# Optimization experiments

Hardware: AMD Instinct MI355X
Metric: run time of the kernel (lower is better)

The kernel has to match this reference:

```python
import jax, jax.numpy as jnp
import numpy as np

B, E, WIN, DX, DZ, RAW = 2048, 32, 10, 14, 14, 22

def _leaky(x):
    return jnp.where(x >= 0, x, 0.01 * x)

def setup_inputs():
    key = jax.random.key(0)
    ks = jax.random.split(key, 20)
    def w(k, i, o):
        return jax.random.normal(k, (i, o), dtype=jnp.float32) / np.float32(np.sqrt(i))
    def b(k, o):
        return jax.random.normal(k, (o,), dtype=jnp.float32) * 0.01
    return {
        "raw_obs": jax.random.normal(ks[0], (B, WIN, 1, RAW), dtype=jnp.float32),
        "state_prev": jax.random.normal(ks[1], (B, E, WIN, DX), dtype=jnp.float32),
        "pm_w1": w(ks[2], WIN * DX, 256), "pm_b1": b(ks[3], 256),
        "pm_w3": w(ks[4], 256, 512), "pm_b3": b(ks[5], 512),
        "pm_wm2": w(ks[6], 512, DX), "pm_bm2": b(ks[7], DX),
        "sm_w2": w(ks[8], WIN * RAW, 256), "sm_b2": b(ks[9], 256),
        "sm_w3": w(ks[10], 256, 256), "sm_b3": b(ks[11], 256),
        "sm_w5": w(ks[12], 256, 64), "sm_b5": b(ks[13], 64),
        "sm_w6": w(ks[14], 64, DZ), "sm_b6": b(ks[15], DZ),
        "on_w1": w(ks[16], DZ, 32), "on_b1": b(ks[17], 32),
        "on_w2": w(ks[18], 32, DZ), "on_b2": b(ks[19], DZ),
    }

def reference(raw_obs, state_prev, pm_w1, pm_b1, pm_w3, pm_b3, pm_wm2, pm_bm2,
              sm_w2, sm_b2, sm_w3, sm_b3, sm_w5, sm_b5, sm_w6, sm_b6,
              on_w1, on_b1, on_w2, on_b2):
    bs, ens, win, dx = state_prev.shape
    dz = sm_w6.shape[1]
    # --- process model (LinearFlipout evaluated at mean weights) ---
    x = state_prev.reshape(bs * ens, win * dx)
    x = _leaky(x @ pm_w1 + pm_b1)
    x = _leaky(x @ pm_w3 + pm_b3)
    state_pred = (x @ pm_wm2 + pm_bm2).reshape(bs, ens, dx)   # [B,E,dx]
    state_m = state_pred.mean(axis=1)                          # [B,dx]
    A = state_pred - state_m[:, None, :]                       # [B,E,dx]
    # --- sensor model: torch repeat(E,1,1,1) tiles ensemble-major, the final
    # reshape reinterprets as batch-major; replicate that layout faithfully ---
    s = jnp.tile(raw_obs, (ens, 1, 1, 1)).reshape(bs * ens, win * raw_obs.shape[-1])
    s = _leaky(s @ sm_w2 + sm_b2)
    s = _leaky(s @ sm_w3 + sm_b3)
    s = _leaky(s @ sm_w5 + sm_b5)
    s = s @ sm_w6 + sm_b6
    ensemble_z = s.reshape(bs, ens, dz)                        # [B,E,dz]
    z = ensemble_z.mean(axis=1, keepdims=True)                 # [B,1,dz]
    # --- observation noise R = diag_embed(square(mlp(z)+c) + init) ---
    r = jax.nn.relu(z @ on_w1 + on_b1) @ on_w2 + on_b2
    r = jnp.square(r + 0.001) + 0.038729833
    R = r.reshape(bs, dz)[:, :, None] * jnp.eye(dz, dtype=r.dtype)  # [B,dz,dz]
    # --- EnKF correction ---
    S = jnp.einsum('bei,bej->bij', A, A)                       # AT @ A, [B,dx,dx]
    innovation = S / (ens - 1) + R
    K = (S / (ens - 1)) @ jnp.linalg.inv(innovation)           # [B,dx,dz]
    diff = ensemble_z - state_pred                             # (y - H_XT)^T, [B,E,dz]
    gain = jnp.einsum('bij,bej->bei', K, diff)                 # [B,E,dx]
    state_corrected = state_pred + gain
    return (state_corrected,
            state_corrected.mean(axis=1, keepdims=True),
            state_m[:, None, :],
            z,
            ensemble_z)
```

## Files before the change

kernel.cpp:

```cpp
#include <hip/hip_runtime.h>

typedef unsigned short u16;
typedef __attribute__((ext_vector_type(8))) short short8;
typedef __attribute__((ext_vector_type(4))) float floatx4;

#define MFMA_BF16 __builtin_amdgcn_mfma_f32_16x16x32_bf16

__device__ __forceinline__ u16 f2bf(float f) {
    union { float f; unsigned int i; } v; v.f = f;
    unsigned int u = v.i;
    u += 0x7fffu + ((u >> 16) & 1u);
    return (u16)(u >> 16);
}
__device__ __forceinline__ float leaky(float x) { return x >= 0.f ? x : 0.01f * x; }

#define H1S 264
#define RS 232
#define H3S 72
#define CS 136

#define O1 917504
#define O2 946176
#define O3 974848
#define O4 1003520

#define PW1   0
#define PW3   40960
#define PWM2  172032
#define PSW2  180224
#define PSW3  237568
#define PSW5  303104
#define PSW6  319488
#define PTOTAL 320512
#define WS_NEEDED 641024
#define WS_BIG (641024 + 3670016)

struct PackSeg { const float* W; int K, N, S, base, count; };
struct PackArgs { PackSeg seg[7]; };

__global__ __launch_bounds__(256) void pack_all(PackArgs pa, u16* __restrict__ P) {
    int u = blockIdx.x * 256 + threadIdx.x;
    if (u >= PTOTAL) return;
#pragma unroll
    for (int i = 0; i < 7; i++) {
        if (u >= pa.seg[i].base && u < pa.seg[i].base + pa.seg[i].count) {
            int v = u - pa.seg[i].base;
            int j = v & 7;
            int l = (v >> 3) & 63;
            int ts = v >> 9;
            int s = ts % pa.seg[i].S;
            int t = ts / pa.seg[i].S;
            int k = s * 32 + (l >> 4) * 8 + j;
            int n = t * 16 + (l & 15);
            P[u] = (k < pa.seg[i].K && n < pa.seg[i].N)
                       ? f2bf(pa.seg[i].W[k * pa.seg[i].N + n]) : (u16)0;
            return;
        }
    }
}

__device__ __forceinline__ short8 load_x_frag(const float* __restrict__ X,
                                              int row, int s, int q) {
    const float* p = X + row * 140;
    float4 v0 = {0.f, 0.f, 0.f, 0.f}, v1 = {0.f, 0.f, 0.f, 0.f};
    int col0 = s * 32 + q * 8;
    if (s < 4) {
        v0 = *(const float4*)(p + col0);
        v1 = *(const float4*)(p + col0 + 4);
    } else {
        if (q <= 1) v0 = *(const float4*)(p + col0);
        if (q == 0) v1 = *(const float4*)(p + col0 + 4);
    }
    short8 r;
    r[0] = (short)f2bf(v0.x); r[1] = (short)f2bf(v0.y);
    r[2] = (short)f2bf(v0.z); r[3] = (short)f2bf(v0.w);
    r[4] = (short)f2bf(v1.x); r[5] = (short)f2bf(v1.y);
    r[6] = (short)f2bf(v1.z); r[7] = (short)f2bf(v1.w);
    return r;
}

__global__ __launch_bounds__(256, 5) void merged_mlp(
    const float* __restrict__ Rg, const float* __restrict__ Xg,
    const u16* __restrict__ Pk,
    const float* __restrict__ b1, const float* __restrict__ b3,
    const float* __restrict__ bm2,
    const float* __restrict__ b2, const float* __restrict__ sb3,
    const float* __restrict__ b5, const float* __restrict__ b6,
    float* __restrict__ ez_out,
    float* __restrict__ sp_ws)
{
    __shared__ __align__(16) u16 ldsH[32 * H1S];
    __shared__ __align__(16) u16 ldsC[32 * CS];

    const int tid  = threadIdx.x;
    const int lane = tid & 63;
    const int wave = tid >> 6;
    const int q    = lane >> 4;
    const int n16  = lane & 15;

    if (blockIdx.x < 64) {
        const u16* w2p = Pk + PSW2;
        const u16* w3p = Pk + PSW3;
        const u16* w5p = Pk + PSW5;
        const u16* w6p = Pk + PSW6;
        const int row0 = blockIdx.x * 32;

        for (int idx = tid; idx < 32 * 56; idx += 256) {
            int r = idx / 56, c4 = idx - r * 56;
            float4 v = {0.f, 0.f, 0.f, 0.f};
            if (c4 < 55) v = *(const float4*)&Rg[(row0 + r) * 220 + c4 * 4];
            u16* dst = &ldsH[r * RS + c4 * 4];
            dst[0] = f2bf(v.x); dst[1] = f2bf(v.y); dst[2] = f2bf(v.z); dst[3] = f2bf(v.w);
        }
        __syncthreads();

        floatx4 acc1[2][4];
        {
            floatx4 zero = {0.f, 0.f, 0.f, 0.f};
            for (int rt = 0; rt < 2; rt++)
                for (int ct = 0; ct < 4; ct++) acc1[rt][ct] = zero;
#pragma unroll
            for (int s = 0; s < 7; s++) {
                short8 a0 = *(const short8*)&ldsH[n16 * RS + s * 32 + q * 8];
                short8 a1 = *(const short8*)&ldsH[(n16 + 16) * RS + s * 32 + q * 8];
#pragma unroll
                for (int ct = 0; ct < 4; ct++) {
                    int t = wave * 4 + ct;
                    short8 bf = *(const short8*)&w2p[((t * 7 + s) * 64 + lane) * 8];
                    acc1[0][ct] = MFMA_BF16(a0, bf, acc1[0][ct], 0, 0, 0);
                    acc1[1][ct] = MFMA_BF16(a1, bf, acc1[1][ct], 0, 0, 0);
                }
            }
        }
        __syncthreads();
#pragma unroll
        for (int ct = 0; ct < 4; ct++) {
            int col = (wave * 4 + ct) * 16 + n16;
            float bias = b2[col];
#pragma unroll
            for (int rt = 0; rt < 2; rt++)
#pragma unroll
                for (int r = 0; r < 4; r++)
                    ldsH[(rt * 16 + q * 4 + r) * H1S + col] = f2bf(leaky(acc1[rt][ct][r] + bias));
        }
        __syncthreads();

        floatx4 acc5[2];
        {
            floatx4 zero = {0.f, 0.f, 0.f, 0.f};
            acc5[0] = zero; acc5[1] = zero;
        }
#pragma unroll
        for (int c = 0; c < 2; c++) {
            floatx4 zero = {0.f, 0.f, 0.f, 0.f};
            floatx4 acc[2][2];
            for (int rt = 0; rt < 2; rt++)
                for (int ct = 0; ct < 2; ct++) acc[rt][ct] = zero;
#pragma unroll
            for (int s = 0; s < 8; s++) {
                short8 a0 = *(const short8*)&ldsH[n16 * H1S + s * 32 + q * 8];
                short8 a1 = *(const short8*)&ldsH[(n16 + 16) * H1S + s * 32 + q * 8];
#pragma unroll
                for (int ct = 0; ct < 2; ct++) {
                    int tg = c * 8 + wave * 2 + ct;
                    short8 bf = *(const short8*)&w3p[((tg * 8 + s) * 64 + lane) * 8];
                    acc[0][ct] = MFMA_BF16(a0, bf, acc[0][ct], 0, 0, 0);
                    acc[1][ct] = MFMA_BF16(a1, bf, acc[1][ct], 0, 0, 0);
                }
            }
#pragma unroll
            for (int ct = 0; ct < 2; ct++) {
                int cl = (wave * 2 + ct) * 16 + n16;
                float bias = sb3[c * 128 + cl];
#pragma unroll
                for (int rt = 0; rt < 2; rt++)
#pragma unroll
                    for (int r = 0; r < 4; r++)
                        ldsC[(rt * 16 + q * 4 + r) * CS + cl] = f2bf(leaky(acc[rt][ct][r] + bias));
            }
            __syncthreads();
#pragma unroll
            for (int sl = 0; sl < 4; sl++) {
                int sg = c * 4 + sl;
                short8 bf = *(const short8*)&w5p[((wave * 8 + sg) * 64 + lane) * 8];
#pragma unroll
                for (int rt = 0; rt < 2; rt++) {
                    short8 a = *(const short8*)&ldsC[(rt * 16 + n16) * CS + sl * 32 + q * 8];
                    acc5[rt] = MFMA_BF16(a, bf, acc5[rt], 0, 0, 0);
                }
            }
            __syncthreads();
        }

        {
            int col = wave * 16 + n16;
            float bias = b5[col];
#pragma unroll
            for (int rt = 0; rt < 2; rt++)
#pragma unroll
                for (int r = 0; r < 4; r++)
                    ldsC[(rt * 16 + q * 4 + r) * H3S + col] = f2bf(leaky(acc5[rt][r] + bias));
        }
        __syncthreads();

        if (wave < 2) {
            floatx4 zero = {0.f, 0.f, 0.f, 0.f};
            floatx4 acc[2] = {zero, zero};
            int s = wave;
            short8 a0 = *(const short8*)&ldsC[n16 * H3S + s * 32 + q * 8];
            short8 a1 = *(const short8*)&ldsC[(n16 + 16) * H3S + s * 32 + q * 8];
            short8 bf = *(const short8*)&w6p[(s * 64 + lane) * 8];
            acc[0] = MFMA_BF16(a0, bf, acc[0], 0, 0, 0);
            acc[1] = MFMA_BF16(a1, bf, acc[1], 0, 0, 0);
            float* pacc = (float*)ldsH;
#pragma unroll
            for (int rt = 0; rt < 2; rt++)
#pragma unroll
                for (int r = 0; r < 4; r++)
                    pacc[(wave * 32 + rt * 16 + q * 4 + r) * 16 + n16] = acc[rt][r];
        }
        __syncthreads();
        {
            const float* pacc = (const float*)ldsH;
            for (int idx = tid; idx < 512; idx += 256) {
                int r = idx >> 4, c = idx & 15;
                float v = pacc[idx] + pacc[512 + idx];
                if (c < 14) ez_out[(row0 + r) * 14 + c] = v + b6[c];
            }
        }
    } else {
        const u16* w1p  = Pk + PW1;
        const u16* w3p  = Pk + PW3;
        const u16* wm2p = Pk + PWM2;
        const int bb   = blockIdx.x - 64;
        const int row0 = bb * 32;

        {
            floatx4 zero = {0.f, 0.f, 0.f, 0.f};
            floatx4 acc[2][4];
            for (int rt = 0; rt < 2; rt++)
                for (int ct = 0; ct < 4; ct++) acc[rt][ct] = zero;
#pragma unroll
            for (int s = 0; s < 5; s++) {
                short8 a0 = load_x_frag(Xg, row0 + n16, s, q);
                short8 a1 = load_x_frag(Xg, row0 + 16 + n16, s, q);
#pragma unroll
                for (int ct = 0; ct < 4; ct++) {
                    int t = wave * 4 + ct;
                    short8 bf = *(const short8*)&w1p[((t * 5 + s) * 64 + lane) * 8];
                    acc[0][ct] = MFMA_BF16(a0, bf, acc[0][ct], 0, 0, 0);
                    acc[1][ct] = MFMA_BF16(a1, bf, acc[1][ct], 0, 0, 0);
                }
            }
#pragma unroll
            for (int ct = 0; ct < 4; ct++) {
                int col = (wave * 4 + ct) * 16 + n16;
                float bias = b1[col];
#pragma unroll
                for (int rt = 0; rt < 2; rt++)
#pragma unroll
                    for (int r = 0; r < 4; r++)
                        ldsH[(rt * 16 + q * 4 + r) * H1S + col] = f2bf(leaky(acc[rt][ct][r] + bias));
            }
        }
        __syncthreads();

        floatx4 acc3[2];
        {
            floatx4 zero = {0.f, 0.f, 0.f, 0.f};
            acc3[0] = zero; acc3[1] = zero;
        }
#pragma unroll
        for (int c = 0; c < 4; c++) {
            floatx4 zero = {0.f, 0.f, 0.f, 0.f};
            floatx4 acc[2][2];
            for (int rt = 0; rt < 2; rt++)
                for (int ct = 0; ct < 2; ct++) acc[rt][ct] = zero;
#pragma unroll
            for (int s = 0; s < 8; s++) {
                short8 a0 = *(const short8*)&ldsH[n16 * H1S + s * 32 + q * 8];
                short8 a1 = *(const short8*)&ldsH[(n16 + 16) * H1S + s * 32 + q * 8];
#pragma unroll
                for (int ct = 0; ct < 2; ct++) {
                    int tg = c * 8 + wave * 2 + ct;
                    short8 bf = *(const short8*)&w3p[((tg * 8 + s) * 64 + lane) * 8];
                    acc[0][ct] = MFMA_BF16(a0, bf, acc[0][ct], 0, 0, 0);
                    acc[1][ct] = MFMA_BF16(a1, bf, acc[1][ct], 0, 0, 0);
                }
            }
#pragma unroll
            for (int ct = 0; ct < 2; ct++) {
                int cl = (wave * 2 + ct) * 16 + n16;
                float bias = b3[c * 128 + cl];
#pragma unroll
                for (int rt = 0; rt < 2; rt++)
#pragma unroll
                    for (int r = 0; r < 4; r++)
                        ldsC[(rt * 16 + q * 4 + r) * CS + cl] = f2bf(leaky(acc[rt][ct][r] + bias));
            }
            __syncthreads();
            {
                int sg = c * 4 + wave;
                short8 bf = *(const short8*)&wm2p[(sg * 64 + lane) * 8];
#pragma unroll
                for (int rt = 0; rt < 2; rt++) {
                    short8 a = *(const short8*)&ldsC[(rt * 16 + n16) * CS + wave * 32 + q * 8];
                    acc3[rt] = MFMA_BF16(a, bf, acc3[rt], 0, 0, 0);
                }
            }
            __syncthreads();
        }

        {
            float* pacc = (float*)ldsH;
#pragma unroll
            for (int rt = 0; rt < 2; rt++)
#pragma unroll
                for (int r = 0; r < 4; r++)
                    pacc[(wave * 32 + rt * 16 + q * 4 + r) * 16 + n16] = acc3[rt][r];
        }
        __syncthreads();
        {
            const float* pacc = (const float*)ldsH;
            for (int idx = tid; idx < 512; idx += 256) {
                int r = idx >> 4, c = idx & 15;
                float v = pacc[idx] + pacc[512 + idx] + pacc[1024 + idx] + pacc[1536 + idx];
                if (c < 14) sp_ws[(row0 + r) * 14 + c] = v + bm2[c];
            }
        }
    }
}

__global__ __launch_bounds__(64) void enkf_tail(
    const float* __restrict__ sp_all,
    const float* __restrict__ on_w1, const float* __restrict__ on_b1,
    const float* __restrict__ on_w2, const float* __restrict__ on_b2,
    float* out)
{
    __shared__ float spv[32][14];
    __shared__ float ezv[32][14];
    __shared__ float smv[14], zzv[14], rrv[14];
    __shared__ float M[14][14], Kmat[14][14];
    __shared__ float G[14][28];
    __shared__ float fac[14];
    __shared__ float hbuf[32];

    const int l = threadIdx.x;
    const int b = blockIdx.x;

    for (int idx = l; idx < 448; idx += 64) ((float*)spv)[idx] = sp_all[b * 448 + idx];
    {
        const float* ezsrc = out + O4 + (b & 63) * 448;
        for (int idx = l; idx < 448; idx += 64) ((float*)ezv)[idx] = ezsrc[idx];
    }

    if (l < 14) {
        float s1 = 0.f, s2 = 0.f;
        for (int e = 0; e < 32; e++) { s1 += spv[e][l]; s2 += ezv[e][l]; }
        smv[l] = s1 * (1.f / 32.f);
        zzv[l] = s2 * (1.f / 32.f);
    }
    if (l < 32) {
        float t = on_b1[l];
        for (int k = 0; k < 14; k++) t += zzv[k] * on_w1[k * 32 + l];
        hbuf[l] = t > 0.f ? t : 0.f;
    }
    if (l < 14) {
        float t = on_b2[l];
        for (int k = 0; k < 32; k++) t += hbuf[k] * on_w2[k * 14 + l];
        t += 0.001f;
        rrv[l] = t * t + 0.038729833f;
    }
    for (int idx = l; idx < 196; idx += 64) {
        int i = idx / 14, j = idx - i * 14;
        float s = 0.f;
        for (int e = 0; e < 32; e++) s += (spv[e][i] - smv[i]) * (spv[e][j] - smv[j]);
        s *= (1.f / 31.f);
        M[i][j] = s;
        G[i][j] = s + (i == j ? rrv[i] : 0.f);
        G[i][14 + j] = (i == j) ? 1.f : 0.f;
    }
    for (int c = 0; c < 14; c++) {
        float pinv = 1.f / G[c][c];
        if (l < 28) G[c][l] *= pinv;
        if (l < 14 && l != c) fac[l] = G[l][c];
        for (int idx = l; idx < 392; idx += 64) {
            int i = idx / 28, j = idx - i * 28;
            if (i != c) G[i][j] -= fac[i] * G[c][j];
        }
    }
    for (int idx = l; idx < 196; idx += 64) {
        int i = idx / 14, j = idx - i * 14;
        float s = 0.f;
        for (int k = 0; k < 14; k++) s += M[i][k] * G[k][14 + j];
        Kmat[i][j] = s;
    }
    for (int idx = l; idx < 448; idx += 64) {
        int e = idx / 14, i = idx - e * 14;
        float g = 0.f;
        for (int j = 0; j < 14; j++) g += Kmat[i][j] * (ezv[e][j] - spv[e][j]);
        out[b * 448 + idx] = spv[e][i] + g;
        out[O4 + b * 448 + idx] = ezv[e][i];
    }
    if (l < 14) {
        float g = 0.f;
        for (int j = 0; j < 14; j++) g += Kmat[l][j] * (zzv[j] - smv[j]);
        out[O1 + b * 14 + l] = smv[l] + g;
        out[O2 + b * 14 + l] = smv[l];
        out[O3 + b * 14 + l] = zzv[l];
    }
}

extern "C" void kernel_launch(void* const* d_in, const int* in_sizes, int n_in,
                              void* d_out, int out_size, void* d_ws, size_t ws_size,
                              hipStream_t stream) {
    (void)in_sizes; (void)n_in; (void)out_size; (void)ws_size;

    const float* raw_obs    = (const float*)d_in[0];
    const float* state_prev = (const float*)d_in[1];
    const float* pm_w1  = (const float*)d_in[2];
    const float* pm_b1  = (const float*)d_in[3];
    const float* pm_w3  = (const float*)d_in[4];
    const float* pm_b3  = (const float*)d_in[5];
    const float* pm_wm2 = (const float*)d_in[6];
    const float* pm_bm2 = (const float*)d_in[7];
    const float* sm_w2  = (const float*)d_in[8];
    const float* sm_b2  = (const float*)d_in[9];
    const float* sm_w3  = (const float*)d_in[10];
    const float* sm_b3  = (const float*)d_in[11];
    const float* sm_w5  = (const float*)d_in[12];
    const float* sm_b5  = (const float*)d_in[13];
    const float* sm_w6  = (const float*)d_in[14];
    const float* sm_b6  = (const float*)d_in[15];
    const float* on_w1  = (const float*)d_in[16];
    const float* on_b1  = (const float*)d_in[17];
    const float* on_w2  = (const float*)d_in[18];
    const float* on_b2  = (const float*)d_in[19];

    float* out = (float*)d_out;
    u16* P = (u16*)d_ws;
    float* sp_ws = (float*)((char*)d_ws + WS_NEEDED);

    PackArgs pa;
    pa.seg[0] = { pm_w1,  140, 256, 5,  PW1,  40960  };
    pa.seg[1] = { pm_w3,  256, 512, 8,  PW3,  131072 };
    pa.seg[2] = { pm_wm2, 512, 14,  16, PWM2, 8192   };
    pa.seg[3] = { sm_w2,  220, 256, 7,  PSW2, 57344  };
    pa.seg[4] = { sm_w3,  256, 256, 8,  PSW3, 65536  };
    pa.seg[5] = { sm_w5,  256, 64,  8,  PSW5, 16384  };
    pa.seg[6] = { sm_w6,  64,  14,  2,  PSW6, 1024   };
    pack_all<<<(PTOTAL + 255) / 256, 256, 0, stream>>>(pa, P);

    merged_mlp<<<2112, 256, 0, stream>>>(raw_obs, state_prev, P,
                                         pm_b1, pm_b3, pm_bm2,
                                         sm_b2, sm_b3, sm_b5, sm_b6,
                                         out + O4, sp_ws);
    enkf_tail<<<2048, 64, 0, stream>>>(sp_ws, on_w1, on_b1, on_w2, on_b2, out);
}
```

Baseline: 183.1 us.

## Widen LDS hidden-layer staging to full width and cut chunk barriers

The intermediate LDS buffer grows to the full 256-wide hidden row. The sensor model's second layer is now computed in one pass, ping-ponging between two buffers, and layer 5 runs as a single K=256 reduction instead of being interleaved over two chunks. The process model's 512-wide layer now uses two 256-column chunks instead of four 128-column chunks, with four column tiles per wave, which halves the barrier count there. In exchange, LDS use and live accumulator registers grow, and the launch-bounds occupancy hint drops from 5 to 4 blocks per CU.

```diff
diff --git a/kernel.cpp b/kernel.cpp
--- a/kernel.cpp
+++ b/kernel.cpp
@@ -17,7 +17,6 @@
 #define H1S 264
 #define RS 232
 #define H3S 72
-#define CS 136
 
 #define O1 917504
 #define O2 946176
@@ -79,7 +78,7 @@
     return r;
 }
 
-__global__ __launch_bounds__(256, 5) void merged_mlp(
+__global__ __launch_bounds__(256, 4) void merged_mlp(
     const float* __restrict__ Rg, const float* __restrict__ Xg,
     const u16* __restrict__ Pk,
     const float* __restrict__ b1, const float* __restrict__ b3,
@@ -90,7 +89,7 @@
     float* __restrict__ sp_ws)
 {
     __shared__ __align__(16) u16 ldsH[32 * H1S];
-    __shared__ __align__(16) u16 ldsC[32 * CS];
+    __shared__ __align__(16) u16 ldsC[32 * H1S];
 
     const int tid  = threadIdx.x;
     const int lane = tid & 63;
@@ -114,11 +113,11 @@
         }
         __syncthreads();
 
-        floatx4 acc1[2][4];
-        {
-            floatx4 zero = {0.f, 0.f, 0.f, 0.f};
-            for (int rt = 0; rt < 2; rt++)
-                for (int ct = 0; ct < 4; ct++) acc1[rt][ct] = zero;
+        {
+            floatx4 zero = {0.f, 0.f, 0.f, 0.f};
+            floatx4 acc[2][4];
+            for (int rt = 0; rt < 2; rt++)
+                for (int ct = 0; ct < 4; ct++) acc[rt][ct] = zero;
 #pragma unroll
             for (int s = 0; s < 7; s++) {
                 short8 a0 = *(const short8*)&ldsH[n16 * RS + s * 32 + q * 8];
@@ -127,79 +126,71 @@
                 for (int ct = 0; ct < 4; ct++) {
                     int t = wave * 4 + ct;
                     short8 bf = *(const short8*)&w2p[((t * 7 + s) * 64 + lane) * 8];
-                    acc1[0][ct] = MFMA_BF16(a0, bf, acc1[0][ct], 0, 0, 0);
-                    acc1[1][ct] = MFMA_BF16(a1, bf, acc1[1][ct], 0, 0, 0);
+                    acc[0][ct] = MFMA_BF16(a0, bf, acc[0][ct], 0, 0, 0);
+                    acc[1][ct] = MFMA_BF16(a1, bf, acc[1][ct], 0, 0, 0);
                 }
             }
-        }
-        __syncthreads();
-#pragma unroll
-        for (int ct = 0; ct < 4; ct++) {
-            int col = (wave * 4 + ct) * 16 + n16;
-            float bias = b2[col];
-#pragma unroll
-            for (int rt = 0; rt < 2; rt++)
-#pragma unroll
-                for (int r = 0; r < 4; r++)
-                    ldsH[(rt * 16 + q * 4 + r) * H1S + col] = f2bf(leaky(acc1[rt][ct][r] + bias));
-        }
-        __syncthreads();
-
-        floatx4 acc5[2];
-        {
-            floatx4 zero = {0.f, 0.f, 0.f, 0.f};
-            acc5[0] = zero; acc5[1] = zero;
-        }
-#pragma unroll
-        for (int c = 0; c < 2; c++) {
-            floatx4 zero = {0.f, 0.f, 0.f, 0.f};
-            floatx4 acc[2][2];
-            for (int rt = 0; rt < 2; rt++)
-                for (int ct = 0; ct < 2; ct++) acc[rt][ct] = zero;
+#pragma unroll
+            for (int ct = 0; ct < 4; ct++) {
+                int col = (wave * 4 + ct) * 16 + n16;
+                float bias = b2[col];
+#pragma unroll
+                for (int rt = 0; rt < 2; rt++)
+#pragma unroll
+                    for (int r = 0; r < 4; r++)
+                        ldsC[(rt * 16 + q * 4 + r) * H1S + col] = f2bf(leaky(acc[rt][ct][r] + bias));
+            }
+        }
+        __syncthreads();
+
+        {
+            floatx4 zero = {0.f, 0.f, 0.f, 0.f};
+            floatx4 acc[2][4];
+            for (int rt = 0; rt < 2; rt++)
+                for (int ct = 0; ct < 4; ct++) acc[rt][ct] = zero;
+#pragma unroll
+            for (int s = 0; s < 8; s++) {
+                short8 a0 = *(const short8*)&ldsC[n16 * H1S + s * 32 + q * 8];
+                short8 a1 = *(const short8*)&ldsC[(n16 + 16) * H1S + s * 32 + q * 8];
+#pragma unroll
+                for (int ct = 0; ct < 4; ct++) {
+                    int t = wave * 4 + ct;
+                    short8 bf = *(const short8*)&w3p[((t * 8 + s) * 64 + lane) * 8];
+                    acc[0][ct] = MFMA_BF16(a0, bf, acc[0][ct], 0, 0, 0);
+                    acc[1][ct] = MFMA_BF16(a1, bf, acc[1][ct], 0, 0, 0);
+                }
+            }
+#pragma unroll
+            for (int ct = 0; ct < 4; ct++) {
+                int col = (wave * 4 + ct) * 16 + n16;
+                float bias = sb3[col];
+#pragma unroll
+                for (int rt = 0; rt < 2; rt++)
+#pragma unroll
+                    for (int r = 0; r < 4; r++)
+                        ldsH[(rt * 16 + q * 4 + r) * H1S + col] = f2bf(leaky(acc[rt][ct][r] + bias));
+            }
+        }
+        __syncthreads();
+
+        {
+            floatx4 zero = {0.f, 0.f, 0.f, 0.f};
+            floatx4 acc[2] = {zero, zero};
 #pragma unroll
             for (int s = 0; s < 8; s++) {
                 short8 a0 = *(const short8*)&ldsH[n16 * H1S + s * 32 + q * 8];
                 short8 a1 = *(const short8*)&ldsH[(n16 + 16) * H1S + s * 32 + q * 8];
-#pragma unroll
-                for (int ct = 0; ct < 2; ct++) {
-                    int tg = c * 8 + wave * 2 + ct;
-                    short8 bf = *(const short8*)&w3p[((tg * 8 + s) * 64 + lane) * 8];
-                    acc[0][ct] = MFMA_BF16(a0, bf, acc[0][ct], 0, 0, 0);
-                    acc[1][ct] = MFMA_BF16(a1, bf, acc[1][ct], 0, 0, 0);
-                }
-            }
-#pragma unroll
-            for (int ct = 0; ct < 2; ct++) {
-                int cl = (wave * 2 + ct) * 16 + n16;
-                float bias = sb3[c * 128 + cl];
-#pragma unroll
-                for (int rt = 0; rt < 2; rt++)
-#pragma unroll
-                    for (int r = 0; r < 4; r++)
-                        ldsC[(rt * 16 + q * 4 + r) * CS + cl] = f2bf(leaky(acc[rt][ct][r] + bias));
-            }
-            __syncthreads();
-#pragma unroll
-            for (int sl = 0; sl < 4; sl++) {
-                int sg = c * 4 + sl;
-                short8 bf = *(const short8*)&w5p[((wave * 8 + sg) * 64 + lane) * 8];
-#pragma unroll
-                for (int rt = 0; rt < 2; rt++) {
-                    short8 a = *(const short8*)&ldsC[(rt * 16 + n16) * CS + sl * 32 + q * 8];
-                    acc5[rt] = MFMA_BF16(a, bf, acc5[rt], 0, 0, 0);
-                }
-            }
-            __syncthreads();
-        }
-
-        {
+                short8 bf = *(const short8*)&w5p[((wave * 8 + s) * 64 + lane) * 8];
+                acc[0] = MFMA_BF16(a0, bf, acc[0], 0, 0, 0);
+                acc[1] = MFMA_BF16(a1, bf, acc[1], 0, 0, 0);
+            }
             int col = wave * 16 + n16;
             float bias = b5[col];
 #pragma unroll
             for (int rt = 0; rt < 2; rt++)
 #pragma unroll
                 for (int r = 0; r < 4; r++)
-                    ldsC[(rt * 16 + q * 4 + r) * H3S + col] = f2bf(leaky(acc5[rt][r] + bias));
+                    ldsC[(rt * 16 + q * 4 + r) * H3S + col] = f2bf(leaky(acc[rt][r] + bias));
         }
         __syncthreads();
 
@@ -271,40 +262,42 @@
             acc3[0] = zero; acc3[1] = zero;
         }
 #pragma unroll
-        for (int c = 0; c < 4; c++) {
-            floatx4 zero = {0.f, 0.f, 0.f, 0.f};
-            floatx4 acc[2][2];
-            for (int rt = 0; rt < 2; rt++)
-                for (int ct = 0; ct < 2; ct++) acc[rt][ct] = zero;
+        for (int c = 0; c < 2; c++) {
+            floatx4 zero = {0.f, 0.f, 0.f, 0.f};
+            floatx4 acc[2][4];
+            for (int rt = 0; rt < 2; rt++)
+                for (int ct = 0; ct < 4; ct++) acc[rt][ct] = zero;
 #pragma unroll
             for (int s = 0; s < 8; s++) {
                 short8 a0 = *(const short8*)&ldsH[n16 * H1S + s * 32 + q * 8];
                 short8 a1 = *(const short8*)&ldsH[(n16 + 16) * H1S + s * 32 + q * 8];
 #pragma unroll
-                for (int ct = 0; ct < 2; ct++) {
-                    int tg = c * 8 + wave * 2 + ct;
+                for (int ct = 0; ct < 4; ct++) {
+                    int tg = c * 16 + wave * 4 + ct;
                     short8 bf = *(const short8*)&w3p[((tg * 8 + s) * 64 + lane) * 8];
                     acc[0][ct] = MFMA_BF16(a0, bf, acc[0][ct], 0, 0, 0);
                     acc[1][ct] = MFMA_BF16(a1, bf, acc[1][ct], 0, 0, 0);
                 }
             }
 #pragma unroll
-            for (int ct = 0; ct < 2; ct++) {
-                int cl = (wave * 2 + ct) * 16 + n16;
-                float bias = b3[c * 128 + cl];
+            for (int ct = 0; ct < 4; ct++) {
+                int cl = (wave * 4 + ct) * 16 + n16;
+                float bias = b3[c * 256 + cl];
 #pragma unroll
                 for (int rt = 0; rt < 2; rt++)
 #pragma unroll
                     for (int r = 0; r < 4; r++)
-                        ldsC[(rt * 16 + q * 4 + r) * CS + cl] = f2bf(leaky(acc[rt][ct][r] + bias));
+                        ldsC[(rt * 16 + q * 4 + r) * H1S + cl] = f2bf(leaky(acc[rt][ct][r] + bias));
             }
             __syncthreads();
-            {
-                int sg = c * 4 + wave;
+#pragma unroll
+            for (int s2 = 0; s2 < 2; s2++) {
+                int sl = wave * 2 + s2;
+                int sg = c * 8 + sl;
                 short8 bf = *(const short8*)&wm2p[(sg * 64 + lane) * 8];
 #pragma unroll
                 for (int rt = 0; rt < 2; rt++) {
-                    short8 a = *(const short8*)&ldsC[(rt * 16 + n16) * CS + wave * 32 + q * 8];
+                    short8 a = *(const short8*)&ldsC[(rt * 16 + n16) * H1S + sl * 32 + q * 8];
                     acc3[rt] = MFMA_BF16(a, bf, acc3[rt], 0, 0, 0);
                 }
             }
@@ -312,7 +305,7 @@
         }
 
         {
-            float* pacc = (float*)ldsH;
+            float* pacc = (float*)ldsC;
 #pragma unroll
             for (int rt = 0; rt < 2; rt++)
 #pragma unroll
@@ -321,7 +314,7 @@
         }
         __syncthreads();
         {
-            const float* pacc = (const float*)ldsH;
+            const float* pacc = (const float*)ldsC;
             for (int idx = tid; idx < 512; idx += 256) {
                 int r = idx >> 4, c = idx & 15;
                 float v = pacc[idx] + pacc[512 + idx] + pacc[1024 + idx] + pacc[1536 + idx];
```

Measured after the change: 186.8 us. 1.02x slower.
